# Performance work log

Hardware: AMD Instinct MI355X
Metric: run time of the kernel (lower is better)

Reference implementation:

```python
import jax, jax.numpy as jnp
import numpy as np

VOCAB = 100000
EMBED = 64
HIDDEN = 256
SEQ = 200
BATCH = 4096


def setup_inputs() -> dict:
    key = jax.random.key(0)
    ks = jax.random.split(key, 12)
    s = 0.02
    return {
        "user_hist": jax.random.randint(ks[0], (BATCH, SEQ), 0, VOCAB),
        "target_item": jax.random.randint(ks[1], (BATCH,), 0, VOCAB),
        "user_emb": jax.random.normal(ks[2], (VOCAB, EMBED), jnp.float32) * s,
        "item_emb": jax.random.normal(ks[3], (VOCAB, EMBED), jnp.float32) * s,
        "attn_w1": jax.random.normal(ks[4], (4 * EMBED, HIDDEN), jnp.float32) * s,
        "attn_b1": jnp.zeros((HIDDEN,), jnp.float32),
        "attn_w2": jax.random.normal(ks[5], (HIDDEN, 1), jnp.float32) * s,
        "attn_b2": jnp.zeros((1,), jnp.float32),
        "mlp_w1": jax.random.normal(ks[6], (2 * EMBED, HIDDEN), jnp.float32) * s,
        "mlp_b1": jnp.zeros((HIDDEN,), jnp.float32),
        "mlp_w2": jax.random.normal(ks[7], (HIDDEN, 1), jnp.float32) * s,
        "mlp_b2": jnp.zeros((1,), jnp.float32),
    }


def reference(user_hist, target_item, user_emb, item_emb,
              attn_w1, attn_b1, attn_w2, attn_b2,
              mlp_w1, mlp_b1, mlp_w2, mlp_b2):
    # [B, S, E] history embeddings, [B, 1, E] target embedding
    h = user_emb[user_hist]
    t = item_emb[target_item][:, None, :]
    tb = jnp.broadcast_to(t, h.shape)
    # attention MLP over [B, S, 4E]
    att_in = jnp.concatenate([h, tb, h - t, h * t], axis=-1)
    att_h = jax.nn.relu(att_in @ attn_w1 + attn_b1)
    att_logits = (att_h @ attn_w2 + attn_b2)[..., 0]            # [B, S]
    att_w = jax.nn.softmax(att_logits, axis=-1)[..., None]      # [B, S, 1]
    user_interest = jnp.sum(h * att_w, axis=1)                  # [B, E]
    # prediction head on [B, 2E]
    mlp_in = jnp.concatenate([user_interest, t[:, 0, :]], axis=-1)
    mlp_h = jax.nn.relu(mlp_in @ mlp_w1 + mlp_b1)
    out = jax.nn.sigmoid(mlp_h @ mlp_w2 + mlp_b2)               # [B, 1]
    return out
```

## Files before the change

### kernel.cpp

```cpp
#include <hip/hip_runtime.h>
#include <math.h>

#define EMBED   64
#define HIDDEN  256
#define SEQ     200
#define SEQP    208
#define MT      13
#define VOCAB   100000

typedef _Float16 f16x8  __attribute__((ext_vector_type(8)));
typedef float    f32x4  __attribute__((ext_vector_type(4)));
typedef float    f32x2  __attribute__((ext_vector_type(2)));


__global__ void din_setup(const float* __restrict__ attn_w1,
                          const float* __restrict__ mlp_w1,
                          const float* __restrict__ user_emb,
                          uint2* __restrict__ fragB8,
                          _Float16* __restrict__ fragW3,
                          _Float16* __restrict__ fragDt,
                          _Float16* __restrict__ fragB2,
                          unsigned char* __restrict__ emb8,
                          int do_emb) {
  const int gid = blockIdx.x * 256 + threadIdx.x;
  if (gid < 2048) {
    const int i = gid >> 7, rem = gid & 127, kc = rem >> 6, lane = rem & 63;
    const int n = i * 16 + (lane & 15);
    const int kb = kc * 32 + (lane >> 4) * 8;
    float v[8];
    #pragma unroll
    for (int j = 0; j < 8; ++j)
      v[j] = 16.0f * (attn_w1[(kb + j) * HIDDEN + n] + attn_w1[(128 + kb + j) * HIDDEN + n]);
    int lo = __builtin_amdgcn_cvt_pk_fp8_f32(v[0], v[1], 0, false);
    lo     = __builtin_amdgcn_cvt_pk_fp8_f32(v[2], v[3], lo, true);
    int hi = __builtin_amdgcn_cvt_pk_fp8_f32(v[4], v[5], 0, false);
    hi     = __builtin_amdgcn_cvt_pk_fp8_f32(v[6], v[7], hi, true);
    fragB8[gid] = uint2{(unsigned)lo, (unsigned)hi};
  } else if (gid < 4096) {
    const int g = gid - 2048;
    const int i = g >> 7, rem = g & 127, kc = rem >> 6, lane = rem & 63;
    const int n = i * 16 + (lane & 15);
    const int kb = kc * 32 + (lane >> 4) * 8;
    #pragma unroll
    for (int j = 0; j < 8; ++j)
      fragW3[g * 8 + j] = (_Float16)(16.0f * attn_w1[(192 + kb + j) * HIDDEN + n]);
  } else if (gid < 6144) {
    const int g = gid - 4096;
    const int i = g >> 7, rem = g & 127, kc = rem >> 6, lane = rem & 63;
    const int n = i * 16 + (lane & 15);
    const int kb = kc * 32 + (lane >> 4) * 8;
    #pragma unroll
    for (int j = 0; j < 8; ++j)
      fragDt[g * 8 + j] = (_Float16)(attn_w1[(64 + kb + j) * HIDDEN + n]
                                   - attn_w1[(128 + kb + j) * HIDDEN + n]);
  } else if (gid < 10240) {
    const int g = gid - 6144;
    const int nt = g >> 8, kc = (g >> 6) & 3, lane = g & 63;
    const int n = nt * 16 + (lane & 15);
    const int kb = kc * 32 + (lane >> 4) * 8;
    #pragma unroll
    for (int j = 0; j < 8; ++j)
      fragB2[g * 8 + j] = (_Float16)mlp_w1[(kb + j) * HIDDEN + n];
  } else if (do_emb) {
    const int g = gid - 10240;
    if (g < VOCAB * EMBED / 8) {
      const int base = g * 8;
      const float4 x = *reinterpret_cast<const float4*>(&user_emb[base]);
      const float4 y = *reinterpret_cast<const float4*>(&user_emb[base + 4]);
      int lo = __builtin_amdgcn_cvt_pk_fp8_f32(16.f * x.x, 16.f * x.y, 0, false);
      lo     = __builtin_amdgcn_cvt_pk_fp8_f32(16.f * x.z, 16.f * x.w, lo, true);
      int hi = __builtin_amdgcn_cvt_pk_fp8_f32(16.f * y.x, 16.f * y.y, 0, false);
      hi     = __builtin_amdgcn_cvt_pk_fp8_f32(16.f * y.z, 16.f * y.w, hi, true);
      *reinterpret_cast<uint2*>(&emb8[base]) = uint2{(unsigned)lo, (unsigned)hi};
    }
  }
}

__global__ __launch_bounds__(512, 8)
void din_fused_kernel(const int* __restrict__ user_hist,
                      const int* __restrict__ target_item,
                      const float* __restrict__ user_emb,
                      const float* __restrict__ item_emb,
                      const float* __restrict__ attn_b1,
                      const float* __restrict__ attn_w2,
                      const float* __restrict__ mlp_b1,
                      const float* __restrict__ mlp_w2,
                      const float* __restrict__ mlp_b2,
                      const uint2* __restrict__ fragB8,
                      const _Float16* __restrict__ fragW3,
                      const _Float16* __restrict__ fragDt,
                      const _Float16* __restrict__ fragB2,
                      const unsigned char* __restrict__ emb8,
                      float* __restrict__ out)
{
  __shared__ __align__(16) uint2 Hf8[MT * 2 * 64];
  __shared__ __align__(16) _Float16 t16[EMBED];
  __shared__ int   histL[SEQP];
  __shared__ float lp[8][SEQP];
  __shared__ float weights[SEQP];
  __shared__ __align__(16) _Float16 mi16[EMBED];
  __shared__ float red[16];

  const int b    = blockIdx.x;
  const int tid  = threadIdx.x;
  const int lane = tid & 63;
  const int wave = tid >> 6;
  const int m    = lane & 15;
  const int quad = lane >> 4;

  if (tid < EMBED) t16[tid] = (_Float16)item_emb[target_item[b] * EMBED + tid];
  if (tid < SEQP) histL[tid] = (tid < SEQ) ? user_hist[b * SEQ + tid] : 0;

  uint2 w8r[2][2];
  #pragma unroll
  for (int i = 0; i < 2; ++i)
    #pragma unroll
    for (int c = 0; c < 2; ++c)
      w8r[i][c] = fragB8[((2 * wave + i) * 2 + c) * 64 + lane];
  __syncthreads();

  if (emb8) {
    for (int slot = tid; slot < MT * 2 * 64; slot += 512) {
      const int ln = slot & 63, kcomb = slot >> 6;
      const int st = kcomb >> 1, kc = kcomb & 1;
      const int s = st * 16 + (ln & 15);
      const int kb = kc * 32 + (ln >> 4) * 8;
      uint2 pv = uint2{0u, 0u};
      if (s < SEQ)
        pv = *reinterpret_cast<const uint2*>(&emb8[histL[s] * EMBED + kb]);
      Hf8[slot] = pv;
    }
  } else {
    for (int slot = tid; slot < MT * 2 * 64; slot += 512) {
      const int ln = slot & 63, kcomb = slot >> 6;
      const int st = kcomb >> 1, kc = kcomb & 1;
      const int s = st * 16 + (ln & 15);
      const int kb = kc * 32 + (ln >> 4) * 8;
      uint2 pv = uint2{0u, 0u};
      if (s < SEQ) {
        const float4* src = reinterpret_cast<const float4*>(&user_emb[histL[s] * EMBED + kb]);
        const float4 x = src[0], y = src[1];
        int lo = __builtin_amdgcn_cvt_pk_fp8_f32(16.f * x.x, 16.f * x.y, 0, false);
        lo     = __builtin_amdgcn_cvt_pk_fp8_f32(16.f * x.z, 16.f * x.w, lo, true);
        int hi = __builtin_amdgcn_cvt_pk_fp8_f32(16.f * y.x, 16.f * y.y, 0, false);
        hi     = __builtin_amdgcn_cvt_pk_fp8_f32(16.f * y.z, 16.f * y.w, hi, true);
        pv = uint2{(unsigned)lo, (unsigned)hi};
      }
      Hf8[slot] = pv;
    }
  }

  const f16x8 tv0 = *reinterpret_cast<const f16x8*>(&t16[quad * 8]);
  const f16x8 tv1 = *reinterpret_cast<const f16x8*>(&t16[32 + quad * 8]);

  long long Aw[2][2];
  #pragma unroll
  for (int i = 0; i < 2; ++i) {
    #pragma unroll
    for (int c = 0; c < 2; ++c) {
      const uint2 w8 = w8r[i][c];
      const f32x2 e0 = __builtin_amdgcn_cvt_pk_f32_fp8((int)w8.x, false);
      const f32x2 e1 = __builtin_amdgcn_cvt_pk_f32_fp8((int)w8.x, true);
      const f32x2 e2 = __builtin_amdgcn_cvt_pk_f32_fp8((int)w8.y, false);
      const f32x2 e3 = __builtin_amdgcn_cvt_pk_f32_fp8((int)w8.y, true);
      const f16x8 w3v = reinterpret_cast<const f16x8*>(fragW3)[((2 * wave + i) * 2 + c) * 64 + lane];
      const f16x8 p = w3v * (c ? tv1 : tv0);
      int lo = __builtin_amdgcn_cvt_pk_fp8_f32(e0.x + (float)p[0], e0.y + (float)p[1], 0, false);
      lo     = __builtin_amdgcn_cvt_pk_fp8_f32(e1.x + (float)p[2], e1.y + (float)p[3], lo, true);
      int hi = __builtin_amdgcn_cvt_pk_fp8_f32(e2.x + (float)p[4], e2.y + (float)p[5], 0, false);
      hi     = __builtin_amdgcn_cvt_pk_fp8_f32(e3.x + (float)p[6], e3.y + (float)p[7], hi, true);
      Aw[i][c] = __builtin_bit_cast(long long, uint2{(unsigned)lo, (unsigned)hi});
    }
  }

  float cn[2][4], w2n[2][4];
  #pragma unroll
  for (int i = 0; i < 2; ++i) {
    const int tile = 2 * wave + i;
    const f16x8 d0 = reinterpret_cast<const f16x8*>(fragDt)[(tile * 2 + 0) * 64 + lane];
    const f16x8 d1 = reinterpret_cast<const f16x8*>(fragDt)[(tile * 2 + 1) * 64 + lane];
    f32x4 acc = {0.f, 0.f, 0.f, 0.f};
    acc = __builtin_amdgcn_mfma_f32_16x16x32_f16(d0, tv0, acc, 0, 0, 0);
    acc = __builtin_amdgcn_mfma_f32_16x16x32_f16(d1, tv1, acc, 0, 0, 0);
    const int nb = tile * 16 + quad * 4;
    const float4 b1v = *reinterpret_cast<const float4*>(&attn_b1[nb]);
    const float4 w2v = *reinterpret_cast<const float4*>(&attn_w2[nb]);
    cn[i][0] = 256.0f * (b1v.x + acc[0]);
    cn[i][1] = 256.0f * (b1v.y + acc[1]);
    cn[i][2] = 256.0f * (b1v.z + acc[2]);
    cn[i][3] = 256.0f * (b1v.w + acc[3]);
    w2n[i][0] = w2v.x * (1.0f / 256.0f);
    w2n[i][1] = w2v.y * (1.0f / 256.0f);
    w2n[i][2] = w2v.z * (1.0f / 256.0f);
    w2n[i][3] = w2v.w * (1.0f / 256.0f);
  }
  __syncthreads();

  #pragma unroll 2
  for (int st = 0; st < MT; ++st) {
    const long long b0 = __builtin_bit_cast(long long, Hf8[(st * 2 + 0) * 64 + lane]);
    const long long b1 = __builtin_bit_cast(long long, Hf8[(st * 2 + 1) * 64 + lane]);
    float lg = 0.f;
    #pragma unroll
    for (int i = 0; i < 2; ++i) {
      f32x4 acc = {cn[i][0], cn[i][1], cn[i][2], cn[i][3]};
      acc = __builtin_amdgcn_mfma_f32_16x16x32_fp8_fp8(Aw[i][0], b0, acc, 0, 0, 0);
      acc = __builtin_amdgcn_mfma_f32_16x16x32_fp8_fp8(Aw[i][1], b1, acc, 0, 0, 0);
      #pragma unroll
      for (int r = 0; r < 4; ++r)
        lg += fmaxf(acc[r], 0.0f) * w2n[i][r];
    }
    lg += __shfl_xor(lg, 16, 64);
    lg += __shfl_xor(lg, 32, 64);
    if (lane < 16) lp[wave][st * 16 + lane] = lg;
  }
  __syncthreads();

  float v = -INFINITY, e = 0.0f;
  if (wave < 4) {
    if (tid < SEQ)
      v = lp[0][tid] + lp[1][tid] + lp[2][tid] + lp[3][tid]
        + lp[4][tid] + lp[5][tid] + lp[6][tid] + lp[7][tid];
    float mx = v;
    #pragma unroll
    for (int off = 32; off; off >>= 1) mx = fmaxf(mx, __shfl_xor(mx, off, 64));
    if (lane == 0) red[wave] = mx;
  }
  __syncthreads();
  if (wave < 4) {
    const float mx = fmaxf(fmaxf(red[0], red[1]), fmaxf(red[2], red[3]));
    e = (tid < SEQ) ? expf(v - mx) : 0.0f;
    float ssum = e;
    #pragma unroll
    for (int off = 32; off; off >>= 1) ssum += __shfl_xor(ssum, off, 64);
    if (lane == 0) red[4 + wave] = ssum;
  }
  __syncthreads();
  if (wave < 4) {
    const float tot = red[4] + red[5] + red[6] + red[7];
    if (tid < SEQP) weights[tid] = (tid < SEQ) ? e / tot : 0.0f;
  }
  __syncthreads();

  {
    const int kc = wave & 1, g = wave >> 1;
    float pk[8];
    #pragma unroll
    for (int j = 0; j < 8; ++j) pk[j] = 0.f;
    #pragma unroll
    for (int st2 = 0; st2 < 4; ++st2) {
      const int st = g + st2 * 4;
      if (st < MT) {
        const float wt = weights[st * 16 + m];
        const uint2 hv = Hf8[(st * 2 + kc) * 64 + lane];
        const f32x2 f0 = __builtin_amdgcn_cvt_pk_f32_fp8((int)hv.x, false);
        const f32x2 f1 = __builtin_amdgcn_cvt_pk_f32_fp8((int)hv.x, true);
        const f32x2 f2 = __builtin_amdgcn_cvt_pk_f32_fp8((int)hv.y, false);
        const f32x2 f3 = __builtin_amdgcn_cvt_pk_f32_fp8((int)hv.y, true);
        pk[0] += wt * f0.x;  pk[1] += wt * f0.y;
        pk[2] += wt * f1.x;  pk[3] += wt * f1.y;
        pk[4] += wt * f2.x;  pk[5] += wt * f2.y;
        pk[6] += wt * f3.x;  pk[7] += wt * f3.y;
      }
    }
    #pragma unroll
    for (int j = 0; j < 8; ++j) {
      float p = pk[j];
      p += __shfl_xor(p, 1, 64);
      p += __shfl_xor(p, 2, 64);
      p += __shfl_xor(p, 4, 64);
      p += __shfl_xor(p, 8, 64);
      pk[j] = p;
    }
    if (m == 0) {
      #pragma unroll
      for (int j = 0; j < 8; ++j)
        lp[g][kc * 32 + quad * 8 + j] = pk[j];
    }
  }
  __syncthreads();
  if (tid < EMBED)
    mi16[tid] = (_Float16)((lp[0][tid] + lp[1][tid] + lp[2][tid] + lp[3][tid]) * 0.0625f);
  __syncthreads();

  {
    const f16x8 mb0 = *reinterpret_cast<const f16x8*>(&mi16[quad * 8]);
    const f16x8 mb1 = *reinterpret_cast<const f16x8*>(&mi16[32 + quad * 8]);
    float z = 0.f;
    #pragma unroll
    for (int i = 0; i < 2; ++i) {
      const f16x8* B2 = reinterpret_cast<const f16x8*>(fragB2) + ((2 * wave + i) * 4) * 64 + lane;
      const int nb = (2 * wave + i) * 16 + quad * 4;
      const float4 bb = *reinterpret_cast<const float4*>(&mlp_b1[nb]);
      const float4 ww = *reinterpret_cast<const float4*>(&mlp_w2[nb]);
      f32x4 acc = {bb.x, bb.y, bb.z, bb.w};
      acc = __builtin_amdgcn_mfma_f32_16x16x32_f16(B2[0],   mb0, acc, 0, 0, 0);
      acc = __builtin_amdgcn_mfma_f32_16x16x32_f16(B2[64],  mb1, acc, 0, 0, 0);
      acc = __builtin_amdgcn_mfma_f32_16x16x32_f16(B2[128], tv0, acc, 0, 0, 0);
      acc = __builtin_amdgcn_mfma_f32_16x16x32_f16(B2[192], tv1, acc, 0, 0, 0);
      z += fmaxf(acc[0], 0.0f) * ww.x;
      z += fmaxf(acc[1], 0.0f) * ww.y;
      z += fmaxf(acc[2], 0.0f) * ww.z;
      z += fmaxf(acc[3], 0.0f) * ww.w;
    }
    z += __shfl_xor(z, 16, 64);
    z += __shfl_xor(z, 32, 64);
    if (lane == 0) red[wave] = z;
  }
  __syncthreads();
  if (tid == 0) {
    const float zz = red[0] + red[1] + red[2] + red[3]
                   + red[4] + red[5] + red[6] + red[7] + mlp_b2[0];
    out[b] = 1.0f / (1.0f + expf(-zz));
  }
}

extern "C" void kernel_launch(void* const* d_in, const int* in_sizes, int n_in,
                              void* d_out, int out_size, void* d_ws, size_t ws_size,
                              hipStream_t stream) {
  const int*   user_hist   = (const int*)  d_in[0];
  const int*   target_item = (const int*)  d_in[1];
  const float* user_emb    = (const float*)d_in[2];
  const float* item_emb    = (const float*)d_in[3];
  const float* attn_w1     = (const float*)d_in[4];
  const float* attn_b1     = (const float*)d_in[5];
  const float* attn_w2     = (const float*)d_in[6];
  const float* mlp_w1      = (const float*)d_in[8];
  const float* mlp_b1      = (const float*)d_in[9];
  const float* mlp_w2      = (const float*)d_in[10];
  const float* mlp_b2      = (const float*)d_in[11];
  float* out = (float*)d_out;

  uint2*    fragB8 = (uint2*)d_ws;
  _Float16* fragW3 = (_Float16*)((char*)d_ws + 16384);
  _Float16* fragDt = (_Float16*)((char*)d_ws + 49152);
  _Float16* fragB2 = (_Float16*)((char*)d_ws + 81920);
  const size_t emb8_off = 147456;
  const size_t emb8_bytes = (size_t)VOCAB * EMBED;
  unsigned char* emb8 = nullptr;
  if (ws_size >= emb8_off + emb8_bytes)
    emb8 = (unsigned char*)d_ws + emb8_off;

  const int setup_gids = 10240 + VOCAB * EMBED / 8;
  din_setup<<<(setup_gids + 255) / 256, 256, 0, stream>>>(
      attn_w1, mlp_w1, user_emb, fragB8, fragW3, fragDt, fragB2,
      emb8 ? emb8 : (unsigned char*)d_ws, emb8 ? 1 : 0);

  const int batch = in_sizes[1];
  din_fused_kernel<<<batch, 512, 0, stream>>>(
      user_hist, target_item, user_emb, item_emb,
      attn_b1, attn_w2, mlp_b1, mlp_w2, mlp_b2,
      fragB8, fragW3, fragDt, fragB2, emb8, out);
}
```

Before: 171.3 us.

## Process two batch rows per block to amortize weight fragment loads

Each 512-thread block now handles two batch rows. The fp8 weight fragments loaded into registers are reused for both rows, and the gather, softmax, pooling and MLP-head phases are split across the two halves of the block. The per-wave logit partials are stored as fp16 so the doubled shared-memory footprint stays small. The cost is more shared memory per block, a serialized per-row attention loop inside each block, and some added precision loss in the logits.

```diff
diff --git a/kernel.cpp b/kernel.cpp
--- a/kernel.cpp
+++ b/kernel.cpp
@@ -91,14 +91,15 @@
                       const _Float16* __restrict__ fragDt,
                       const _Float16* __restrict__ fragB2,
                       const unsigned char* __restrict__ emb8,
-                      float* __restrict__ out)
+                      float* __restrict__ out,
+                      int batch)
 {
-  __shared__ __align__(16) uint2 Hf8[MT * 2 * 64];
-  __shared__ __align__(16) _Float16 t16[EMBED];
-  __shared__ int   histL[SEQP];
-  __shared__ float lp[8][SEQP];
-  __shared__ float weights[SEQP];
-  __shared__ __align__(16) _Float16 mi16[EMBED];
+  __shared__ __align__(16) uint2 Hf8[2][MT * 2 * 64];
+  __shared__ __align__(16) _Float16 lp16[2][8][SEQP];
+  __shared__ int   histL[2][SEQP];
+  __shared__ float weights[2][SEQP];
+  __shared__ __align__(16) _Float16 t16[2][EMBED];
+  __shared__ __align__(16) _Float16 mi16[2][EMBED];
   __shared__ float red[16];
 
   const int b    = blockIdx.x;
@@ -107,9 +108,20 @@
   const int wave = tid >> 6;
   const int m    = lane & 15;
   const int quad = lane >> 4;
-
-  if (tid < EMBED) t16[tid] = (_Float16)item_emb[target_item[b] * EMBED + tid];
-  if (tid < SEQP) histL[tid] = (tid < SEQ) ? user_hist[b * SEQ + tid] : 0;
+  const int bA   = 2 * b;
+  const int bB   = (2 * b + 1 < batch) ? (2 * b + 1) : (2 * b);
+
+  if (tid < 2 * EMBED) {
+    const int r = tid >> 6, e = tid & 63;
+    const int row = r ? bB : bA;
+    t16[r][e] = (_Float16)item_emb[target_item[row] * EMBED + e];
+  }
+  if (tid < SEQP)
+    histL[0][tid] = (tid < SEQ) ? user_hist[bA * SEQ + tid] : 0;
+  if (tid >= 256 && tid < 256 + SEQP) {
+    const int s = tid - 256;
+    histL[1][s] = (s < SEQ) ? user_hist[bB * SEQ + s] : 0;
+  }
 
   uint2 w8r[2][2];
   #pragma unroll
@@ -120,25 +132,29 @@
   __syncthreads();
 
   if (emb8) {
-    for (int slot = tid; slot < MT * 2 * 64; slot += 512) {
+    for (int slot = tid; slot < 2 * MT * 2 * 64; slot += 512) {
       const int ln = slot & 63, kcomb = slot >> 6;
-      const int st = kcomb >> 1, kc = kcomb & 1;
-      const int s = st * 16 + (ln & 15);
+      const int r  = (kcomb >= MT * 2) ? 1 : 0;
+      const int kk = kcomb - r * (MT * 2);
+      const int st = kk >> 1, kc = kk & 1;
+      const int s  = st * 16 + (ln & 15);
       const int kb = kc * 32 + (ln >> 4) * 8;
       uint2 pv = uint2{0u, 0u};
       if (s < SEQ)
-        pv = *reinterpret_cast<const uint2*>(&emb8[histL[s] * EMBED + kb]);
-      Hf8[slot] = pv;
+        pv = *reinterpret_cast<const uint2*>(&emb8[histL[r][s] * EMBED + kb]);
+      Hf8[r][kk * 64 + ln] = pv;
     }
   } else {
-    for (int slot = tid; slot < MT * 2 * 64; slot += 512) {
+    for (int slot = tid; slot < 2 * MT * 2 * 64; slot += 512) {
       const int ln = slot & 63, kcomb = slot >> 6;
-      const int st = kcomb >> 1, kc = kcomb & 1;
-      const int s = st * 16 + (ln & 15);
+      const int r  = (kcomb >= MT * 2) ? 1 : 0;
+      const int kk = kcomb - r * (MT * 2);
+      const int st = kk >> 1, kc = kk & 1;
+      const int s  = st * 16 + (ln & 15);
       const int kb = kc * 32 + (ln >> 4) * 8;
       uint2 pv = uint2{0u, 0u};
       if (s < SEQ) {
-        const float4* src = reinterpret_cast<const float4*>(&user_emb[histL[s] * EMBED + kb]);
+        const float4* src = reinterpret_cast<const float4*>(&user_emb[histL[r][s] * EMBED + kb]);
         const float4 x = src[0], y = src[1];
         int lo = __builtin_amdgcn_cvt_pk_fp8_f32(16.f * x.x, 16.f * x.y, 0, false);
         lo     = __builtin_amdgcn_cvt_pk_fp8_f32(16.f * x.z, 16.f * x.w, lo, true);
@@ -146,113 +162,129 @@
         hi     = __builtin_amdgcn_cvt_pk_fp8_f32(16.f * y.z, 16.f * y.w, hi, true);
         pv = uint2{(unsigned)lo, (unsigned)hi};
       }
-      Hf8[slot] = pv;
-    }
-  }
-
-  const f16x8 tv0 = *reinterpret_cast<const f16x8*>(&t16[quad * 8]);
-  const f16x8 tv1 = *reinterpret_cast<const f16x8*>(&t16[32 + quad * 8]);
-
-  long long Aw[2][2];
+      Hf8[r][kk * 64 + ln] = pv;
+    }
+  }
+
+  float w2n[2][4];
   #pragma unroll
   for (int i = 0; i < 2; ++i) {
-    #pragma unroll
-    for (int c = 0; c < 2; ++c) {
-      const uint2 w8 = w8r[i][c];
-      const f32x2 e0 = __builtin_amdgcn_cvt_pk_f32_fp8((int)w8.x, false);
-      const f32x2 e1 = __builtin_amdgcn_cvt_pk_f32_fp8((int)w8.x, true);
-      const f32x2 e2 = __builtin_amdgcn_cvt_pk_f32_fp8((int)w8.y, false);
-      const f32x2 e3 = __builtin_amdgcn_cvt_pk_f32_fp8((int)w8.y, true);
-      const f16x8 w3v = reinterpret_cast<const f16x8*>(fragW3)[((2 * wave + i) * 2 + c) * 64 + lane];
-      const f16x8 p = w3v * (c ? tv1 : tv0);
-      int lo = __builtin_amdgcn_cvt_pk_fp8_f32(e0.x + (float)p[0], e0.y + (float)p[1], 0, false);
-      lo     = __builtin_amdgcn_cvt_pk_fp8_f32(e1.x + (float)p[2], e1.y + (float)p[3], lo, true);
-      int hi = __builtin_amdgcn_cvt_pk_fp8_f32(e2.x + (float)p[4], e2.y + (float)p[5], 0, false);
-      hi     = __builtin_amdgcn_cvt_pk_fp8_f32(e3.x + (float)p[6], e3.y + (float)p[7], hi, true);
-      Aw[i][c] = __builtin_bit_cast(long long, uint2{(unsigned)lo, (unsigned)hi});
-    }
-  }
-
-  float cn[2][4], w2n[2][4];
-  #pragma unroll
-  for (int i = 0; i < 2; ++i) {
-    const int tile = 2 * wave + i;
-    const f16x8 d0 = reinterpret_cast<const f16x8*>(fragDt)[(tile * 2 + 0) * 64 + lane];
-    const f16x8 d1 = reinterpret_cast<const f16x8*>(fragDt)[(tile * 2 + 1) * 64 + lane];
-    f32x4 acc = {0.f, 0.f, 0.f, 0.f};
-    acc = __builtin_amdgcn_mfma_f32_16x16x32_f16(d0, tv0, acc, 0, 0, 0);
-    acc = __builtin_amdgcn_mfma_f32_16x16x32_f16(d1, tv1, acc, 0, 0, 0);
-    const int nb = tile * 16 + quad * 4;
-    const float4 b1v = *reinterpret_cast<const float4*>(&attn_b1[nb]);
-    const float4 w2v = *reinterpret_cast<const float4*>(&attn_w2[nb]);
-    cn[i][0] = 256.0f * (b1v.x + acc[0]);
-    cn[i][1] = 256.0f * (b1v.y + acc[1]);
-    cn[i][2] = 256.0f * (b1v.z + acc[2]);
-    cn[i][3] = 256.0f * (b1v.w + acc[3]);
+    const float4 w2v = *reinterpret_cast<const float4*>(&attn_w2[(2 * wave + i) * 16 + quad * 4]);
     w2n[i][0] = w2v.x * (1.0f / 256.0f);
     w2n[i][1] = w2v.y * (1.0f / 256.0f);
     w2n[i][2] = w2v.z * (1.0f / 256.0f);
     w2n[i][3] = w2v.w * (1.0f / 256.0f);
   }
-  __syncthreads();
-
-  #pragma unroll 2
-  for (int st = 0; st < MT; ++st) {
-    const long long b0 = __builtin_bit_cast(long long, Hf8[(st * 2 + 0) * 64 + lane]);
-    const long long b1 = __builtin_bit_cast(long long, Hf8[(st * 2 + 1) * 64 + lane]);
-    float lg = 0.f;
+
+  #pragma unroll 1
+  for (int r = 0; r < 2; ++r) {
+    const f16x8 tv0 = *reinterpret_cast<const f16x8*>(&t16[r][quad * 8]);
+    const f16x8 tv1 = *reinterpret_cast<const f16x8*>(&t16[r][32 + quad * 8]);
+
+    long long Aw[2][2];
     #pragma unroll
     for (int i = 0; i < 2; ++i) {
-      f32x4 acc = {cn[i][0], cn[i][1], cn[i][2], cn[i][3]};
-      acc = __builtin_amdgcn_mfma_f32_16x16x32_fp8_fp8(Aw[i][0], b0, acc, 0, 0, 0);
-      acc = __builtin_amdgcn_mfma_f32_16x16x32_fp8_fp8(Aw[i][1], b1, acc, 0, 0, 0);
       #pragma unroll
-      for (int r = 0; r < 4; ++r)
-        lg += fmaxf(acc[r], 0.0f) * w2n[i][r];
-    }
-    lg += __shfl_xor(lg, 16, 64);
-    lg += __shfl_xor(lg, 32, 64);
-    if (lane < 16) lp[wave][st * 16 + lane] = lg;
-  }
-  __syncthreads();
-
+      for (int c = 0; c < 2; ++c) {
+        const uint2 w8 = w8r[i][c];
+        const f32x2 e0 = __builtin_amdgcn_cvt_pk_f32_fp8((int)w8.x, false);
+        const f32x2 e1 = __builtin_amdgcn_cvt_pk_f32_fp8((int)w8.x, true);
+        const f32x2 e2 = __builtin_amdgcn_cvt_pk_f32_fp8((int)w8.y, false);
+        const f32x2 e3 = __builtin_amdgcn_cvt_pk_f32_fp8((int)w8.y, true);
+        const f16x8 w3v = reinterpret_cast<const f16x8*>(fragW3)[((2 * wave + i) * 2 + c) * 64 + lane];
+        const f16x8 p = w3v * (c ? tv1 : tv0);
+        int lo = __builtin_amdgcn_cvt_pk_fp8_f32(e0.x + (float)p[0], e0.y + (float)p[1], 0, false);
+        lo     = __builtin_amdgcn_cvt_pk_fp8_f32(e1.x + (float)p[2], e1.y + (float)p[3], lo, true);
+        int hi = __builtin_amdgcn_cvt_pk_fp8_f32(e2.x + (float)p[4], e2.y + (float)p[5], 0, false);
+        hi     = __builtin_amdgcn_cvt_pk_fp8_f32(e3.x + (float)p[6], e3.y + (float)p[7], hi, true);
+        Aw[i][c] = __builtin_bit_cast(long long, uint2{(unsigned)lo, (unsigned)hi});
+      }
+    }
+
+    float cn[2][4];
+    #pragma unroll
+    for (int i = 0; i < 2; ++i) {
+      const int tile = 2 * wave + i;
+      const f16x8 d0 = reinterpret_cast<const f16x8*>(fragDt)[(tile * 2 + 0) * 64 + lane];
+      const f16x8 d1 = reinterpret_cast<const f16x8*>(fragDt)[(tile * 2 + 1) * 64 + lane];
+      f32x4 acc = {0.f, 0.f, 0.f, 0.f};
+      acc = __builtin_amdgcn_mfma_f32_16x16x32_f16(d0, tv0, acc, 0, 0, 0);
+      acc = __builtin_amdgcn_mfma_f32_16x16x32_f16(d1, tv1, acc, 0, 0, 0);
+      const int nb = tile * 16 + quad * 4;
+      const float4 b1v = *reinterpret_cast<const float4*>(&attn_b1[nb]);
+      cn[i][0] = 256.0f * (b1v.x + acc[0]);
+      cn[i][1] = 256.0f * (b1v.y + acc[1]);
+      cn[i][2] = 256.0f * (b1v.z + acc[2]);
+      cn[i][3] = 256.0f * (b1v.w + acc[3]);
+    }
+
+    if (r == 0) __syncthreads();
+
+    #pragma unroll 2
+    for (int st = 0; st < MT; ++st) {
+      const long long b0 = __builtin_bit_cast(long long, Hf8[r][(st * 2 + 0) * 64 + lane]);
+      const long long b1 = __builtin_bit_cast(long long, Hf8[r][(st * 2 + 1) * 64 + lane]);
+      float lg = 0.f;
+      #pragma unroll
+      for (int i = 0; i < 2; ++i) {
+        f32x4 acc = {cn[i][0], cn[i][1], cn[i][2], cn[i][3]};
+        acc = __builtin_amdgcn_mfma_f32_16x16x32_fp8_fp8(Aw[i][0], b0, acc, 0, 0, 0);
+        acc = __builtin_amdgcn_mfma_f32_16x16x32_fp8_fp8(Aw[i][1], b1, acc, 0, 0, 0);
+        #pragma unroll
+        for (int q = 0; q < 4; ++q)
+          lg += fmaxf(acc[q], 0.0f) * w2n[i][q];
+      }
+      lg += __shfl_xor(lg, 16, 64);
+      lg += __shfl_xor(lg, 32, 64);
+      if (lane < 16) lp16[r][wave][st * 16 + lane] = (_Float16)lg;
+    }
+  }
+  __syncthreads();
+
+  const int r4  = tid >> 8;
+  const int pos = tid & 255;
   float v = -INFINITY, e = 0.0f;
-  if (wave < 4) {
-    if (tid < SEQ)
-      v = lp[0][tid] + lp[1][tid] + lp[2][tid] + lp[3][tid]
-        + lp[4][tid] + lp[5][tid] + lp[6][tid] + lp[7][tid];
+  if (pos < SEQ) {
+    float s = 0.f;
+    #pragma unroll
+    for (int w = 0; w < 8; ++w) s += (float)lp16[r4][w][pos];
+    v = s;
+  }
+  {
     float mx = v;
     #pragma unroll
     for (int off = 32; off; off >>= 1) mx = fmaxf(mx, __shfl_xor(mx, off, 64));
     if (lane == 0) red[wave] = mx;
   }
   __syncthreads();
-  if (wave < 4) {
-    const float mx = fmaxf(fmaxf(red[0], red[1]), fmaxf(red[2], red[3]));
-    e = (tid < SEQ) ? expf(v - mx) : 0.0f;
+  {
+    const float mrow = fmaxf(fmaxf(red[4 * r4 + 0], red[4 * r4 + 1]),
+                             fmaxf(red[4 * r4 + 2], red[4 * r4 + 3]));
+    e = (pos < SEQ) ? expf(v - mrow) : 0.0f;
     float ssum = e;
     #pragma unroll
     for (int off = 32; off; off >>= 1) ssum += __shfl_xor(ssum, off, 64);
-    if (lane == 0) red[4 + wave] = ssum;
-  }
-  __syncthreads();
-  if (wave < 4) {
-    const float tot = red[4] + red[5] + red[6] + red[7];
-    if (tid < SEQP) weights[tid] = (tid < SEQ) ? e / tot : 0.0f;
-  }
-  __syncthreads();
-
-  {
-    const int kc = wave & 1, g = wave >> 1;
+    if (lane == 0) red[8 + wave] = ssum;
+  }
+  __syncthreads();
+  {
+    const float tot = red[8 + 4 * r4 + 0] + red[8 + 4 * r4 + 1]
+                    + red[8 + 4 * r4 + 2] + red[8 + 4 * r4 + 3];
+    if (pos < SEQP) weights[r4][pos] = (pos < SEQ) ? e / tot : 0.0f;
+  }
+  __syncthreads();
+
+  {
+    const int r = wave >> 2, kc = wave & 1, g2 = (wave >> 1) & 1;
     float pk[8];
     #pragma unroll
     for (int j = 0; j < 8; ++j) pk[j] = 0.f;
     #pragma unroll
-    for (int st2 = 0; st2 < 4; ++st2) {
-      const int st = g + st2 * 4;
+    for (int st2 = 0; st2 < 7; ++st2) {
+      const int st = g2 + 2 * st2;
       if (st < MT) {
-        const float wt = weights[st * 16 + m];
-        const uint2 hv = Hf8[(st * 2 + kc) * 64 + lane];
+        const float wt = weights[r][st * 16 + m];
+        const uint2 hv = Hf8[r][(st * 2 + kc) * 64 + lane];
         const f32x2 f0 = __builtin_amdgcn_cvt_pk_f32_fp8((int)hv.x, false);
         const f32x2 f1 = __builtin_amdgcn_cvt_pk_f32_fp8((int)hv.x, true);
         const f32x2 f2 = __builtin_amdgcn_cvt_pk_f32_fp8((int)hv.y, false);
@@ -273,31 +305,39 @@
       pk[j] = p;
     }
     if (m == 0) {
+      float* ip = reinterpret_cast<float*>(&lp16[0][0][0]);
       #pragma unroll
       for (int j = 0; j < 8; ++j)
-        lp[g][kc * 32 + quad * 8 + j] = pk[j];
-    }
-  }
-  __syncthreads();
-  if (tid < EMBED)
-    mi16[tid] = (_Float16)((lp[0][tid] + lp[1][tid] + lp[2][tid] + lp[3][tid]) * 0.0625f);
-  __syncthreads();
-
-  {
-    const f16x8 mb0 = *reinterpret_cast<const f16x8*>(&mi16[quad * 8]);
-    const f16x8 mb1 = *reinterpret_cast<const f16x8*>(&mi16[32 + quad * 8]);
+        ip[((r << 1) + g2) * 64 + kc * 32 + quad * 8 + j] = pk[j];
+    }
+  }
+  __syncthreads();
+  if (tid < 2 * EMBED) {
+    const int r = tid >> 6, e2 = tid & 63;
+    const float* ip = reinterpret_cast<const float*>(&lp16[0][0][0]);
+    mi16[r][e2] = (_Float16)((ip[(2 * r) * 64 + e2] + ip[(2 * r + 1) * 64 + e2]) * 0.0625f);
+  }
+  __syncthreads();
+
+  {
+    const int r = wave >> 2, sub = wave & 3;
+    const f16x8 mb0 = *reinterpret_cast<const f16x8*>(&mi16[r][quad * 8]);
+    const f16x8 mb1 = *reinterpret_cast<const f16x8*>(&mi16[r][32 + quad * 8]);
+    const f16x8 tw0 = *reinterpret_cast<const f16x8*>(&t16[r][quad * 8]);
+    const f16x8 tw1 = *reinterpret_cast<const f16x8*>(&t16[r][32 + quad * 8]);
     float z = 0.f;
     #pragma unroll
-    for (int i = 0; i < 2; ++i) {
-      const f16x8* B2 = reinterpret_cast<const f16x8*>(fragB2) + ((2 * wave + i) * 4) * 64 + lane;
-      const int nb = (2 * wave + i) * 16 + quad * 4;
+    for (int i = 0; i < 4; ++i) {
+      const int tt = sub * 4 + i;
+      const f16x8* B2 = reinterpret_cast<const f16x8*>(fragB2) + (tt * 4) * 64 + lane;
+      const int nb = tt * 16 + quad * 4;
       const float4 bb = *reinterpret_cast<const float4*>(&mlp_b1[nb]);
       const float4 ww = *reinterpret_cast<const float4*>(&mlp_w2[nb]);
       f32x4 acc = {bb.x, bb.y, bb.z, bb.w};
       acc = __builtin_amdgcn_mfma_f32_16x16x32_f16(B2[0],   mb0, acc, 0, 0, 0);
       acc = __builtin_amdgcn_mfma_f32_16x16x32_f16(B2[64],  mb1, acc, 0, 0, 0);
-      acc = __builtin_amdgcn_mfma_f32_16x16x32_f16(B2[128], tv0, acc, 0, 0, 0);
-      acc = __builtin_amdgcn_mfma_f32_16x16x32_f16(B2[192], tv1, acc, 0, 0, 0);
+      acc = __builtin_amdgcn_mfma_f32_16x16x32_f16(B2[128], tw0, acc, 0, 0, 0);
+      acc = __builtin_amdgcn_mfma_f32_16x16x32_f16(B2[192], tw1, acc, 0, 0, 0);
       z += fmaxf(acc[0], 0.0f) * ww.x;
       z += fmaxf(acc[1], 0.0f) * ww.y;
       z += fmaxf(acc[2], 0.0f) * ww.z;
@@ -309,9 +349,11 @@
   }
   __syncthreads();
   if (tid == 0) {
-    const float zz = red[0] + red[1] + red[2] + red[3]
-                   + red[4] + red[5] + red[6] + red[7] + mlp_b2[0];
-    out[b] = 1.0f / (1.0f + expf(-zz));
+    const float zz = red[0] + red[1] + red[2] + red[3] + mlp_b2[0];
+    out[bA] = 1.0f / (1.0f + expf(-zz));
+  } else if (tid == 256 && 2 * b + 1 < batch) {
+    const float zz = red[4] + red[5] + red[6] + red[7] + mlp_b2[0];
+    out[2 * b + 1] = 1.0f / (1.0f + expf(-zz));
   }
 }
 
@@ -347,8 +389,8 @@
       emb8 ? emb8 : (unsigned char*)d_ws, emb8 ? 1 : 0);
 
   const int batch = in_sizes[1];
-  din_fused_kernel<<<batch, 512, 0, stream>>>(
+  din_fused_kernel<<<(batch + 1) / 2, 512, 0, stream>>>(
       user_hist, target_item, user_emb, item_emb,
       attn_b1, attn_w2, mlp_b1, mlp_w2, mlp_b2,
-      fragB8, fragW3, fragDt, fragB2, emb8, out);
+      fragB8, fragW3, fragDt, fragB2, emb8, out, batch);
 }
```

Result: slower. 265.1 us (+54.8%).

## Halve block size to 256 threads with each wave covering four hidden tiles

Applied to the files above, without the earlier changes.

Cuts the fused kernel from 512 to 256 threads per block. Each of the four waves now processes four hidden tiles in two passes, accumulating logits in shared memory, and the pooling and prediction-head work is redistributed to match. The intent is to drop idle waves in the softmax and reduction phases, shrink shared memory, and let more blocks share a CU. In exchange each wave does more serial MFMA work and runs a second pass over the history tiles.

```diff
diff --git a/kernel.cpp b/kernel.cpp
--- a/kernel.cpp
+++ b/kernel.cpp
@@ -76,7 +76,7 @@
   }
 }
 
-__global__ __launch_bounds__(512, 8)
+__global__ __launch_bounds__(256, 6)
 void din_fused_kernel(const int* __restrict__ user_hist,
                       const int* __restrict__ target_item,
                       const float* __restrict__ user_emb,
@@ -94,12 +94,12 @@
                       float* __restrict__ out)
 {
   __shared__ __align__(16) uint2 Hf8[MT * 2 * 64];
+  __shared__ float lpf[4][SEQP];
+  __shared__ int   histL[SEQP];
+  __shared__ float weights[SEQP];
   __shared__ __align__(16) _Float16 t16[EMBED];
-  __shared__ int   histL[SEQP];
-  __shared__ float lp[8][SEQP];
-  __shared__ float weights[SEQP];
   __shared__ __align__(16) _Float16 mi16[EMBED];
-  __shared__ float red[16];
+  __shared__ float red[8];
 
   const int b    = blockIdx.x;
   const int tid  = threadIdx.x;
@@ -110,17 +110,10 @@
 
   if (tid < EMBED) t16[tid] = (_Float16)item_emb[target_item[b] * EMBED + tid];
   if (tid < SEQP) histL[tid] = (tid < SEQ) ? user_hist[b * SEQ + tid] : 0;
-
-  uint2 w8r[2][2];
-  #pragma unroll
-  for (int i = 0; i < 2; ++i)
-    #pragma unroll
-    for (int c = 0; c < 2; ++c)
-      w8r[i][c] = fragB8[((2 * wave + i) * 2 + c) * 64 + lane];
   __syncthreads();
 
   if (emb8) {
-    for (int slot = tid; slot < MT * 2 * 64; slot += 512) {
+    for (int slot = tid; slot < MT * 2 * 64; slot += 256) {
       const int ln = slot & 63, kcomb = slot >> 6;
       const int st = kcomb >> 1, kc = kcomb & 1;
       const int s = st * 16 + (ln & 15);
@@ -131,7 +124,7 @@
       Hf8[slot] = pv;
     }
   } else {
-    for (int slot = tid; slot < MT * 2 * 64; slot += 512) {
+    for (int slot = tid; slot < MT * 2 * 64; slot += 256) {
       const int ln = slot & 63, kcomb = slot >> 6;
       const int st = kcomb >> 1, kc = kcomb & 1;
       const int s = st * 16 + (ln & 15);
@@ -153,81 +146,83 @@
   const f16x8 tv0 = *reinterpret_cast<const f16x8*>(&t16[quad * 8]);
   const f16x8 tv1 = *reinterpret_cast<const f16x8*>(&t16[32 + quad * 8]);
 
-  long long Aw[2][2];
-  #pragma unroll
-  for (int i = 0; i < 2; ++i) {
-    #pragma unroll
-    for (int c = 0; c < 2; ++c) {
-      const uint2 w8 = w8r[i][c];
-      const f32x2 e0 = __builtin_amdgcn_cvt_pk_f32_fp8((int)w8.x, false);
-      const f32x2 e1 = __builtin_amdgcn_cvt_pk_f32_fp8((int)w8.x, true);
-      const f32x2 e2 = __builtin_amdgcn_cvt_pk_f32_fp8((int)w8.y, false);
-      const f32x2 e3 = __builtin_amdgcn_cvt_pk_f32_fp8((int)w8.y, true);
-      const f16x8 w3v = reinterpret_cast<const f16x8*>(fragW3)[((2 * wave + i) * 2 + c) * 64 + lane];
-      const f16x8 p = w3v * (c ? tv1 : tv0);
-      int lo = __builtin_amdgcn_cvt_pk_fp8_f32(e0.x + (float)p[0], e0.y + (float)p[1], 0, false);
-      lo     = __builtin_amdgcn_cvt_pk_fp8_f32(e1.x + (float)p[2], e1.y + (float)p[3], lo, true);
-      int hi = __builtin_amdgcn_cvt_pk_fp8_f32(e2.x + (float)p[4], e2.y + (float)p[5], 0, false);
-      hi     = __builtin_amdgcn_cvt_pk_fp8_f32(e3.x + (float)p[6], e3.y + (float)p[7], hi, true);
-      Aw[i][c] = __builtin_bit_cast(long long, uint2{(unsigned)lo, (unsigned)hi});
-    }
-  }
-
-  float cn[2][4], w2n[2][4];
-  #pragma unroll
-  for (int i = 0; i < 2; ++i) {
-    const int tile = 2 * wave + i;
-    const f16x8 d0 = reinterpret_cast<const f16x8*>(fragDt)[(tile * 2 + 0) * 64 + lane];
-    const f16x8 d1 = reinterpret_cast<const f16x8*>(fragDt)[(tile * 2 + 1) * 64 + lane];
-    f32x4 acc = {0.f, 0.f, 0.f, 0.f};
-    acc = __builtin_amdgcn_mfma_f32_16x16x32_f16(d0, tv0, acc, 0, 0, 0);
-    acc = __builtin_amdgcn_mfma_f32_16x16x32_f16(d1, tv1, acc, 0, 0, 0);
-    const int nb = tile * 16 + quad * 4;
-    const float4 b1v = *reinterpret_cast<const float4*>(&attn_b1[nb]);
-    const float4 w2v = *reinterpret_cast<const float4*>(&attn_w2[nb]);
-    cn[i][0] = 256.0f * (b1v.x + acc[0]);
-    cn[i][1] = 256.0f * (b1v.y + acc[1]);
-    cn[i][2] = 256.0f * (b1v.z + acc[2]);
-    cn[i][3] = 256.0f * (b1v.w + acc[3]);
-    w2n[i][0] = w2v.x * (1.0f / 256.0f);
-    w2n[i][1] = w2v.y * (1.0f / 256.0f);
-    w2n[i][2] = w2v.z * (1.0f / 256.0f);
-    w2n[i][3] = w2v.w * (1.0f / 256.0f);
-  }
-  __syncthreads();
-
-  #pragma unroll 2
-  for (int st = 0; st < MT; ++st) {
-    const long long b0 = __builtin_bit_cast(long long, Hf8[(st * 2 + 0) * 64 + lane]);
-    const long long b1 = __builtin_bit_cast(long long, Hf8[(st * 2 + 1) * 64 + lane]);
-    float lg = 0.f;
+  #pragma unroll 1
+  for (int p = 0; p < 2; ++p) {
+    long long Aw[2][2];
+    float cn[2][4], w2n[2][4];
     #pragma unroll
     for (int i = 0; i < 2; ++i) {
-      f32x4 acc = {cn[i][0], cn[i][1], cn[i][2], cn[i][3]};
-      acc = __builtin_amdgcn_mfma_f32_16x16x32_fp8_fp8(Aw[i][0], b0, acc, 0, 0, 0);
-      acc = __builtin_amdgcn_mfma_f32_16x16x32_fp8_fp8(Aw[i][1], b1, acc, 0, 0, 0);
+      const int tile = wave * 4 + p * 2 + i;
       #pragma unroll
-      for (int r = 0; r < 4; ++r)
-        lg += fmaxf(acc[r], 0.0f) * w2n[i][r];
-    }
-    lg += __shfl_xor(lg, 16, 64);
-    lg += __shfl_xor(lg, 32, 64);
-    if (lane < 16) lp[wave][st * 16 + lane] = lg;
+      for (int c = 0; c < 2; ++c) {
+        const uint2 w8 = fragB8[(tile * 2 + c) * 64 + lane];
+        const f32x2 e0 = __builtin_amdgcn_cvt_pk_f32_fp8((int)w8.x, false);
+        const f32x2 e1 = __builtin_amdgcn_cvt_pk_f32_fp8((int)w8.x, true);
+        const f32x2 e2 = __builtin_amdgcn_cvt_pk_f32_fp8((int)w8.y, false);
+        const f32x2 e3 = __builtin_amdgcn_cvt_pk_f32_fp8((int)w8.y, true);
+        const f16x8 w3v = reinterpret_cast<const f16x8*>(fragW3)[(tile * 2 + c) * 64 + lane];
+        const f16x8 pp = w3v * (c ? tv1 : tv0);
+        int lo = __builtin_amdgcn_cvt_pk_fp8_f32(e0.x + (float)pp[0], e0.y + (float)pp[1], 0, false);
+        lo     = __builtin_amdgcn_cvt_pk_fp8_f32(e1.x + (float)pp[2], e1.y + (float)pp[3], lo, true);
+        int hi = __builtin_amdgcn_cvt_pk_fp8_f32(e2.x + (float)pp[4], e2.y + (float)pp[5], 0, false);
+        hi     = __builtin_amdgcn_cvt_pk_fp8_f32(e3.x + (float)pp[6], e3.y + (float)pp[7], hi, true);
+        Aw[i][c] = __builtin_bit_cast(long long, uint2{(unsigned)lo, (unsigned)hi});
+      }
+      const f16x8 d0 = reinterpret_cast<const f16x8*>(fragDt)[(tile * 2 + 0) * 64 + lane];
+      const f16x8 d1 = reinterpret_cast<const f16x8*>(fragDt)[(tile * 2 + 1) * 64 + lane];
+      f32x4 acc = {0.f, 0.f, 0.f, 0.f};
+      acc = __builtin_amdgcn_mfma_f32_16x16x32_f16(d0, tv0, acc, 0, 0, 0);
+      acc = __builtin_amdgcn_mfma_f32_16x16x32_f16(d1, tv1, acc, 0, 0, 0);
+      const int nb = tile * 16 + quad * 4;
+      const float4 b1v = *reinterpret_cast<const float4*>(&attn_b1[nb]);
+      const float4 w2v = *reinterpret_cast<const float4*>(&attn_w2[nb]);
+      cn[i][0] = 256.0f * (b1v.x + acc[0]);
+      cn[i][1] = 256.0f * (b1v.y + acc[1]);
+      cn[i][2] = 256.0f * (b1v.z + acc[2]);
+      cn[i][3] = 256.0f * (b1v.w + acc[3]);
+      w2n[i][0] = w2v.x * (1.0f / 256.0f);
+      w2n[i][1] = w2v.y * (1.0f / 256.0f);
+      w2n[i][2] = w2v.z * (1.0f / 256.0f);
+      w2n[i][3] = w2v.w * (1.0f / 256.0f);
+    }
+
+    if (p == 0) __syncthreads();
+
+    #pragma unroll 2
+    for (int st = 0; st < MT; ++st) {
+      const long long b0 = __builtin_bit_cast(long long, Hf8[(st * 2 + 0) * 64 + lane]);
+      const long long b1 = __builtin_bit_cast(long long, Hf8[(st * 2 + 1) * 64 + lane]);
+      float lg = 0.f;
+      #pragma unroll
+      for (int i = 0; i < 2; ++i) {
+        f32x4 acc = {cn[i][0], cn[i][1], cn[i][2], cn[i][3]};
+        acc = __builtin_amdgcn_mfma_f32_16x16x32_fp8_fp8(Aw[i][0], b0, acc, 0, 0, 0);
+        acc = __builtin_amdgcn_mfma_f32_16x16x32_fp8_fp8(Aw[i][1], b1, acc, 0, 0, 0);
+        #pragma unroll
+        for (int q = 0; q < 4; ++q)
+          lg += fmaxf(acc[q], 0.0f) * w2n[i][q];
+      }
+      lg += __shfl_xor(lg, 16, 64);
+      lg += __shfl_xor(lg, 32, 64);
+      if (lane < 16) {
+        if (p == 0) lpf[wave][st * 16 + lane] = lg;
+        else        lpf[wave][st * 16 + lane] += lg;
+      }
+    }
   }
   __syncthreads();
 
   float v = -INFINITY, e = 0.0f;
-  if (wave < 4) {
-    if (tid < SEQ)
-      v = lp[0][tid] + lp[1][tid] + lp[2][tid] + lp[3][tid]
-        + lp[4][tid] + lp[5][tid] + lp[6][tid] + lp[7][tid];
+  if (tid < SEQ)
+    v = lpf[0][tid] + lpf[1][tid] + lpf[2][tid] + lpf[3][tid];
+  {
     float mx = v;
     #pragma unroll
     for (int off = 32; off; off >>= 1) mx = fmaxf(mx, __shfl_xor(mx, off, 64));
     if (lane == 0) red[wave] = mx;
   }
   __syncthreads();
-  if (wave < 4) {
+  {
     const float mx = fmaxf(fmaxf(red[0], red[1]), fmaxf(red[2], red[3]));
     e = (tid < SEQ) ? expf(v - mx) : 0.0f;
     float ssum = e;
@@ -236,20 +231,20 @@
     if (lane == 0) red[4 + wave] = ssum;
   }
   __syncthreads();
-  if (wave < 4) {
+  {
     const float tot = red[4] + red[5] + red[6] + red[7];
     if (tid < SEQP) weights[tid] = (tid < SEQ) ? e / tot : 0.0f;
   }
   __syncthreads();
 
   {
-    const int kc = wave & 1, g = wave >> 1;
+    const int kc = wave & 1, g2 = wave >> 1;
     float pk[8];
     #pragma unroll
     for (int j = 0; j < 8; ++j) pk[j] = 0.f;
     #pragma unroll
-    for (int st2 = 0; st2 < 4; ++st2) {
-      const int st = g + st2 * 4;
+    for (int st2 = 0; st2 < 7; ++st2) {
+      const int st = g2 + 2 * st2;
       if (st < MT) {
         const float wt = weights[st * 16 + m];
         const uint2 hv = Hf8[(st * 2 + kc) * 64 + lane];
@@ -273,14 +268,17 @@
       pk[j] = p;
     }
     if (m == 0) {
+      float* ip = &lpf[0][0];
       #pragma unroll
       for (int j = 0; j < 8; ++j)
-        lp[g][kc * 32 + quad * 8 + j] = pk[j];
-    }
-  }
-  __syncthreads();
-  if (tid < EMBED)
-    mi16[tid] = (_Float16)((lp[0][tid] + lp[1][tid] + lp[2][tid] + lp[3][tid]) * 0.0625f);
+        ip[g2 * 64 + kc * 32 + quad * 8 + j] = pk[j];
+    }
+  }
+  __syncthreads();
+  if (tid < EMBED) {
+    const float* ip = &lpf[0][0];
+    mi16[tid] = (_Float16)((ip[tid] + ip[64 + tid]) * 0.0625f);
+  }
   __syncthreads();
 
   {
@@ -288,9 +286,10 @@
     const f16x8 mb1 = *reinterpret_cast<const f16x8*>(&mi16[32 + quad * 8]);
     float z = 0.f;
     #pragma unroll
-    for (int i = 0; i < 2; ++i) {
-      const f16x8* B2 = reinterpret_cast<const f16x8*>(fragB2) + ((2 * wave + i) * 4) * 64 + lane;
-      const int nb = (2 * wave + i) * 16 + quad * 4;
+    for (int i = 0; i < 4; ++i) {
+      const int tt = wave * 4 + i;
+      const f16x8* B2 = reinterpret_cast<const f16x8*>(fragB2) + (tt * 4) * 64 + lane;
+      const int nb = tt * 16 + quad * 4;
       const float4 bb = *reinterpret_cast<const float4*>(&mlp_b1[nb]);
       const float4 ww = *reinterpret_cast<const float4*>(&mlp_w2[nb]);
       f32x4 acc = {bb.x, bb.y, bb.z, bb.w};
@@ -309,8 +308,7 @@
   }
   __syncthreads();
   if (tid == 0) {
-    const float zz = red[0] + red[1] + red[2] + red[3]
-                   + red[4] + red[5] + red[6] + red[7] + mlp_b2[0];
+    const float zz = red[0] + red[1] + red[2] + red[3] + mlp_b2[0];
     out[b] = 1.0f / (1.0f + expf(-zz));
   }
 }
@@ -347,7 +345,7 @@
       emb8 ? emb8 : (unsigned char*)d_ws, emb8 ? 1 : 0);
 
   const int batch = in_sizes[1];
-  din_fused_kernel<<<batch, 512, 0, stream>>>(
+  din_fused_kernel<<<batch, 256, 0, stream>>>(
       user_hist, target_item, user_emb, item_emb,
       attn_b1, attn_w2, mlp_b1, mlp_w2, mlp_b2,
       fragB8, fragW3, fragDt, fragB2, emb8, out);
```

New measurement: 169.0 us. No clear change (-1.3%).
